# Kernel optimization log

Measured on AMD Instinct MI355X. Metric: run time of the kernel, lower is better.

Reference implementation:

```python
import jax, jax.numpy as jnp
import numpy as np


def setup_inputs() -> dict:
    key = jax.random.key(0)
    k1, k2, k3 = jax.random.split(key, 3)
    B, D, L = 16384, 1024, 4
    x = jax.random.normal(k1, (B, D), dtype=jnp.float32)
    weights = jax.random.normal(k2, (L, D, 1), dtype=jnp.float32)
    biases = jax.random.normal(k3, (L, D, 1), dtype=jnp.float32)
    return {"x": x, "weights": weights, "biases": biases}


def reference(x, weights, biases):
    # DCN cross layer. Literal torch math per layer:
    #   out = (x[:,:,None] @ out[:,None,:] @ w_i + b_i).squeeze(-1) + out
    # Algebraically identical (associativity of matmul):
    #   out = x * (out @ w_i) + b_i.T + out
    w = weights[..., 0]  # (L, D)
    b = biases[..., 0]   # (L, D)

    def step(out, wb):
        w_i, b_i = wb
        s = out @ w_i  # (B,) scalar per row: out . w_i
        out = x * s[:, None] + b_i[None, :] + out
        return out, None

    out, _ = jax.lax.scan(step, x, (w, b))
    return out
```

## Files before the change

kernel.cpp:

```cpp
#include <hip/hip_runtime.h>


typedef float v4f __attribute__((ext_vector_type(4)));

constexpr int D  = 1024;
constexpr int D4 = D / 4;
constexpr int L  = 4;
constexpr int WAVES_PER_BLOCK = 4;
constexpr int ROWS_PER_WAVE   = 4;
constexpr int ROWS_PER_BLOCK  = WAVES_PER_BLOCK * ROWS_PER_WAVE;

__global__ __launch_bounds__(256) void cross_layer_kernel(
    const float* __restrict__ x,
    const float* __restrict__ w,
    const float* __restrict__ b,
    float* __restrict__ out,
    int B)
{
    __shared__ v4f sw [L * D4];
    __shared__ v4f spb[L * D4];

    const int tid = threadIdx.x;

    const v4f* w4 = reinterpret_cast<const v4f*>(w);
    const v4f* b4 = reinterpret_cast<const v4f*>(b);
    #pragma unroll
    for (int l = 0; l < L; ++l)
        sw[l * D4 + tid] = w4[l * D4 + tid];
    {
        v4f p = (v4f)(0.f);
        #pragma unroll
        for (int l = 0; l < L; ++l) {
            p += b4[l * D4 + tid];
            spb[l * D4 + tid] = p;
        }
    }
    __syncthreads();

    const int lane = tid & 63;
    const int wave = tid >> 6;

    v4f wr[L][4];
    #pragma unroll
    for (int l = 0; l < L; ++l)
        #pragma unroll
        for (int c = 0; c < 4; ++c)
            wr[l][c] = sw[l * D4 + lane + c * 64];

    v4f csum[4];
    #pragma unroll
    for (int c = 0; c < 4; ++c)
        csum[c] = spb[(L - 1) * D4 + lane + c * 64];

    float e[3];
    #pragma unroll
    for (int l = 1; l < L; ++l) {
        float part = 0.f;
        #pragma unroll
        for (int c = 0; c < 4; ++c) {
            v4f pb = spb[(l - 1) * D4 + lane + c * 64];
            v4f pr = pb * wr[l][c];
            part += pr.x + pr.y + pr.z + pr.w;
        }
        e[l - 1] = part;
    }
    #pragma unroll
    for (int off = 32; off >= 1; off >>= 1) {
        #pragma unroll
        for (int k = 0; k < 3; ++k)
            e[k] += __shfl_xor(e[k], off, 64);
    }

    const int row0 = blockIdx.x * ROWS_PER_BLOCK + wave * ROWS_PER_WAVE;
    #pragma unroll
    for (int r = 0; r < ROWS_PER_WAVE; ++r) {
        const int row = row0 + r;
        if (row >= B) break;

        const v4f* x4 = reinterpret_cast<const v4f*>(x + (size_t)row * D);
        v4f xr[4];
        #pragma unroll
        for (int c = 0; c < 4; ++c)
            xr[c] = __builtin_nontemporal_load(&x4[lane + c * 64]);

        float dd[4];
        #pragma unroll
        for (int l = 0; l < L; ++l) {
            v4f acc = xr[0] * wr[l][0];
            #pragma unroll
            for (int c = 1; c < 4; ++c)
                acc += xr[c] * wr[l][c];
            dd[l] = acc.x + acc.y + acc.z + acc.w;
        }
        #pragma unroll
        for (int off = 32; off >= 1; off >>= 1) {
            #pragma unroll
            for (int k = 0; k < 4; ++k)
                dd[k] += __shfl_xor(dd[k], off, 64);
        }

        float A = 1.f + dd[0];
        A = A + A * dd[1] + e[0];
        A = A + A * dd[2] + e[1];
        A = A + A * dd[3] + e[2];

        v4f* o4 = reinterpret_cast<v4f*>(out + (size_t)row * D);
        #pragma unroll
        for (int c = 0; c < 4; ++c) {
            v4f v = xr[c] * A + csum[c];
            __builtin_nontemporal_store(v, &o4[lane + c * 64]);
        }
    }
}

extern "C" void kernel_launch(void* const* d_in, const int* in_sizes, int n_in,
                              void* d_out, int out_size, void* d_ws, size_t ws_size,
                              hipStream_t stream) {
    const float* x  = (const float*)d_in[0];
    const float* w  = (const float*)d_in[1];
    const float* b  = (const float*)d_in[2];
    float* out      = (float*)d_out;

    const int B = in_sizes[0] / D;
    const int blocks = (B + ROWS_PER_BLOCK - 1) / ROWS_PER_BLOCK;
    cross_layer_kernel<<<blocks, 256, 0, stream>>>(x, w, b, out, B);
}
```

Before: 122.5 us.

## Prefetch all wave rows before smem setup and batch reductions with DPP

```diff
diff --git a/kernel.cpp b/kernel.cpp
--- a/kernel.cpp
+++ b/kernel.cpp
@@ -9,8 +9,27 @@
 constexpr int WAVES_PER_BLOCK = 4;
 constexpr int ROWS_PER_WAVE   = 4;
 constexpr int ROWS_PER_BLOCK  = WAVES_PER_BLOCK * ROWS_PER_WAVE;
+constexpr int NRED = 4 * L + 3;
 
-__global__ __launch_bounds__(256) void cross_layer_kernel(
+template<int CTRL>
+__device__ __forceinline__ float dpp_add(float v) {
+    int t = __builtin_amdgcn_update_dpp(0, __float_as_int(v), CTRL, 0xF, 0xF, true);
+    return v + __int_as_float(t);
+}
+
+__device__ __forceinline__ float wave_sum(float v) {
+    v = dpp_add<0x111>(v);
+    v = dpp_add<0x112>(v);
+    v = dpp_add<0x114>(v);
+    v = dpp_add<0x118>(v);
+    v = dpp_add<0x142>(v);
+    v = dpp_add<0x143>(v);
+    return __int_as_float(__builtin_amdgcn_readlane(__float_as_int(v), 63));
+}
+
+__device__ __forceinline__ float hsum(v4f a) { return (a.x + a.y) + (a.z + a.w); }
+
+__global__ __launch_bounds__(256, 4) void cross_layer_kernel(
     const float* __restrict__ x,
     const float* __restrict__ w,
     const float* __restrict__ b,
@@ -20,95 +39,94 @@
     __shared__ v4f sw [L * D4];
     __shared__ v4f spb[L * D4];
 
-    const int tid = threadIdx.x;
+    const int tid  = threadIdx.x;
+    const int lane = tid & 63;
+    const int wave = tid >> 6;
+    const int row0 = blockIdx.x * ROWS_PER_BLOCK + wave * ROWS_PER_WAVE;
 
     const v4f* w4 = reinterpret_cast<const v4f*>(w);
     const v4f* b4 = reinterpret_cast<const v4f*>(b);
+    v4f wt[L], bt[L];
     #pragma unroll
-    for (int l = 0; l < L; ++l)
-        sw[l * D4 + tid] = w4[l * D4 + tid];
+    for (int l = 0; l < L; ++l) wt[l] = w4[l * D4 + tid];
+    #pragma unroll
+    for (int l = 0; l < L; ++l) bt[l] = b4[l * D4 + tid];
+
+    v4f xr[ROWS_PER_WAVE][4];
+    const v4f* x4 = reinterpret_cast<const v4f*>(x) + (size_t)row0 * D4;
+    #pragma unroll
+    for (int r = 0; r < ROWS_PER_WAVE; ++r) {
+        if (row0 + r < B) {
+            #pragma unroll
+            for (int c = 0; c < 4; ++c)
+                xr[r][c] = __builtin_nontemporal_load(&x4[r * D4 + lane + c * 64]);
+        } else {
+            #pragma unroll
+            for (int c = 0; c < 4; ++c) xr[r][c] = (v4f)(0.f);
+        }
+    }
+
     {
         v4f p = (v4f)(0.f);
         #pragma unroll
         for (int l = 0; l < L; ++l) {
-            p += b4[l * D4 + tid];
+            sw[l * D4 + tid] = wt[l];
+            p += bt[l];
             spb[l * D4 + tid] = p;
         }
     }
     __syncthreads();
 
-    const int lane = tid & 63;
-    const int wave = tid >> 6;
-
-    v4f wr[L][4];
+    float red[NRED];
     #pragma unroll
-    for (int l = 0; l < L; ++l)
+    for (int l = 0; l < L; ++l) {
+        v4f wl[4];
         #pragma unroll
         for (int c = 0; c < 4; ++c)
-            wr[l][c] = sw[l * D4 + lane + c * 64];
+            wl[c] = sw[l * D4 + lane + c * 64];
 
-    v4f csum[4];
-    #pragma unroll
-    for (int c = 0; c < 4; ++c)
-        csum[c] = spb[(L - 1) * D4 + lane + c * 64];
+        if (l >= 1) {
+            v4f ea = spb[(l - 1) * D4 + lane] * wl[0];
+            #pragma unroll
+            for (int c = 1; c < 4; ++c)
+                ea += spb[(l - 1) * D4 + lane + c * 64] * wl[c];
+            red[4 * L + l - 1] = hsum(ea);
+        }
 
-    float e[3];
-    #pragma unroll
-    for (int l = 1; l < L; ++l) {
-        float part = 0.f;
         #pragma unroll
-        for (int c = 0; c < 4; ++c) {
-            v4f pb = spb[(l - 1) * D4 + lane + c * 64];
-            v4f pr = pb * wr[l][c];
-            part += pr.x + pr.y + pr.z + pr.w;
+        for (int r = 0; r < ROWS_PER_WAVE; ++r) {
+            v4f a = xr[r][0] * wl[0];
+            #pragma unroll
+            for (int c = 1; c < 4; ++c)
+                a += xr[r][c] * wl[c];
+            red[r * 4 + l] = hsum(a);
         }
-        e[l - 1] = part;
-    }
-    #pragma unroll
-    for (int off = 32; off >= 1; off >>= 1) {
-        #pragma unroll
-        for (int k = 0; k < 3; ++k)
-            e[k] += __shfl_xor(e[k], off, 64);
     }
 
-    const int row0 = blockIdx.x * ROWS_PER_BLOCK + wave * ROWS_PER_WAVE;
+    #pragma unroll
+    for (int k = 0; k < NRED; ++k)
+        red[k] = wave_sum(red[k]);
+
+    float A[ROWS_PER_WAVE];
     #pragma unroll
     for (int r = 0; r < ROWS_PER_WAVE; ++r) {
-        const int row = row0 + r;
-        if (row >= B) break;
+        float a = 1.f + red[r * 4 + 0];
+        a = a + a * red[r * 4 + 1] + red[4 * L + 0];
+        a = a + a * red[r * 4 + 2] + red[4 * L + 1];
+        a = a + a * red[r * 4 + 3] + red[4 * L + 2];
+        A[r] = a;
+    }
 
-        const v4f* x4 = reinterpret_cast<const v4f*>(x + (size_t)row * D);
-        v4f xr[4];
+    v4f* o4 = reinterpret_cast<v4f*>(out) + (size_t)row0 * D4;
+    #pragma unroll
+    for (int c = 0; c < 4; ++c) {
+        const v4f cs = spb[(L - 1) * D4 + lane + c * 64];
         #pragma unroll
-        for (int c = 0; c < 4; ++c)
-            xr[c] = __builtin_nontemporal_load(&x4[lane + c * 64]);
-
-        float dd[4];
-        #pragma unroll
-        for (int l = 0; l < L; ++l) {
-            v4f acc = xr[0] * wr[l][0];
-            #pragma unroll
-            for (int c = 1; c < 4; ++c)
-                acc += xr[c] * wr[l][c];
-            dd[l] = acc.x + acc.y + acc.z + acc.w;
-        }
-        #pragma unroll
-        for (int off = 32; off >= 1; off >>= 1) {
-            #pragma unroll
-            for (int k = 0; k < 4; ++k)
-                dd[k] += __shfl_xor(dd[k], off, 64);
-        }
-
-        float A = 1.f + dd[0];
-        A = A + A * dd[1] + e[0];
-        A = A + A * dd[2] + e[1];
-        A = A + A * dd[3] + e[2];
-
-        v4f* o4 = reinterpret_cast<v4f*>(out + (size_t)row * D);
-        #pragma unroll
-        for (int c = 0; c < 4; ++c) {
-            v4f v = xr[c] * A + csum[c];
-            __builtin_nontemporal_store(v, &o4[lane + c * 64]);
+        for (int r = 0; r < ROWS_PER_WAVE; ++r) {
+            if (row0 + r < B) {
+                v4f v = xr[r][c] * A[r] + cs;
+                __builtin_nontemporal_store(v, &o4[r * D4 + lane + c * 64]);
+            }
         }
     }
 }
```

Result: no change. 123.3 us (+0.6%).
